# Kernel tuning notes

Measured on AMD Instinct MI355X. Metric: run time of the kernel, lower is better.

Reference implementation:

```python
import jax, jax.numpy as jnp
import numpy as np

N = 100000; E = 200000; H = 64; P2 = 250000; P3 = 500000; G = 2048; NC = 10
NF = 18; EF = 18; Y = 0.25; EPS_BN = 1e-5


def setup_inputs() -> dict:
    key = jax.random.key(0)
    ks = jax.random.split(key, 20)
    def rn(i, shape, s=0.05):
        return jax.random.normal(ks[i], shape, jnp.float32) * s
    inp = {}
    inp["x"] = jax.random.normal(ks[0], (N, NF), jnp.float32)
    inp["edge_attr"] = jax.random.normal(ks[1], (E, EF), jnp.float32)
    inp["paths2"] = jax.random.randint(ks[2], (P2, 2), 0, N, jnp.int32)
    inp["ei2"] = jax.random.randint(ks[3], (P2, 1), 0, E, jnp.int32)
    inp["paths3"] = jax.random.randint(ks[4], (P3, 3), 0, N, jnp.int32)
    inp["ei3"] = jax.random.randint(ks[5], (P3, 2), 0, E, jnp.int32)
    inp["batch"] = jnp.sort(jax.random.randint(ks[6], (N,), 0, G, jnp.int32))
    inp["w_feat"] = rn(7, (NF, H)); inp["b_feat"] = jnp.zeros((H,), jnp.float32)
    inp["w_bond"] = rn(8, (EF, H)); inp["b_bond"] = jnp.zeros((H,), jnp.float32)
    inp["w_ih"] = rn(9, (4 * H, 2 * H)); inp["w_hh"] = rn(10, (4 * H, H))
    inp["b_ih"] = jnp.zeros((4 * H,), jnp.float32); inp["b_hh"] = jnp.zeros((4 * H,), jnp.float32)
    inp["bn_g"] = jnp.ones((2, H), jnp.float32); inp["bn_b"] = jnp.zeros((2, H), jnp.float32)
    inp["mlp_w1"] = rn(11, (2, H, H)); inp["mlp_b1"] = jnp.zeros((2, H), jnp.float32)
    inp["bn1_g"] = jnp.ones((2, H), jnp.float32); inp["bn1_b"] = jnp.zeros((2, H), jnp.float32)
    inp["mlp_w2"] = rn(12, (2, H, H)); inp["mlp_b2"] = jnp.zeros((2, H), jnp.float32)
    inp["bn2_g"] = jnp.ones((2, H), jnp.float32); inp["bn2_b"] = jnp.zeros((2, H), jnp.float32)
    inp["w_att"] = rn(13, (H,)); inp["b_att"] = jnp.zeros((1,), jnp.float32)
    inp["w_l1"] = rn(14, (H, H)); inp["b_l1"] = jnp.zeros((H,), jnp.float32)
    inp["w_l2"] = rn(15, (H, NC)); inp["b_l2"] = jnp.zeros((NC,), jnp.float32)
    return inp


def _batch_norm(x, g, b):
    # training-mode BN: biased batch statistics, eps=1e-5 (torch BatchNorm1d)
    m = x.mean(axis=0)
    v = x.var(axis=0)
    return (x - m) * jax.lax.rsqrt(v + EPS_BN) * g + b


def _lstm_final(x_seq, w_ih, w_hh, b_ih, b_hh):
    # x_seq: [P, L, 2H]; torch LSTM gate order i,f,g,o; return final hidden [P, H]
    P = x_seq.shape[0]
    Hd = w_hh.shape[1]
    def step(carry, xt):
        h, c = carry
        gates = xt @ w_ih.T + b_ih + h @ w_hh.T + b_hh
        i, f, g, o = jnp.split(gates, 4, axis=-1)
        c = jax.nn.sigmoid(f) * c + jax.nn.sigmoid(i) * jnp.tanh(g)
        h = jax.nn.sigmoid(o) * jnp.tanh(c)
        return (h, c), None
    h0 = jnp.zeros((P, Hd), x_seq.dtype)
    (h, _), _ = jax.lax.scan(step, (h0, h0), jnp.swapaxes(x_seq, 0, 1))
    return h


def _conv(i, x_in, ea_enc, paths, ei, w_ih, w_hh, b_ih, b_hh, bn_g, bn_b,
          mlp_w1, mlp_b1, bn1_g, bn1_b, mlp_w2, mlp_b2, bn2_g, bn2_b):
    P = paths.shape[0]
    ea = ea_enc[ei]                                        # [P, L-1, H]
    ea = jnp.concatenate([jnp.zeros((P, 1, H), ea.dtype), ea], axis=1)  # [P, L, H]
    x_cat = jnp.concatenate([x_in[paths], ea], axis=-1)    # [P, L, 2H]
    h = _lstm_final(x_cat, w_ih, w_hh, b_ih, b_hh)         # [P, H]
    h = jax.ops.segment_sum(h, paths[:, -1], num_segments=N)  # scatter_add to nodes
    h = _batch_norm(h, bn_g[i], bn_b[i])                   # residuals=False
    h = jax.nn.relu(_batch_norm(h @ mlp_w1[i] + mlp_b1[i], bn1_g[i], bn1_b[i]))
    h = jax.nn.relu(_batch_norm(h @ mlp_w2[i] + mlp_b2[i], bn2_g[i], bn2_b[i]))
    return h


def _attention(query, keys, w_att, b_att):
    scores = []
    for k in keys:
        s = jnp.sum(query * k, axis=0)                     # [H], sum over nodes
        s = (s - s.min()) / (s.max() - s.min() + 1e-6)
        scores.append(s @ w_att + b_att[0])                # scalar
    w = jax.nn.softmax(jnp.stack(scores))                  # [K]
    rep = sum(k * w[j] for j, k in enumerate(keys))
    return rep + query


def _forward(x, edge_attr, w_feat, b_feat, w_bond, b_bond, w_ih, w_hh, b_ih, b_hh,
             bn_g, bn_b, mlp_w1, mlp_b1, bn1_g, bn1_b, mlp_w2, mlp_b2, bn2_g, bn2_b,
             w_att, b_att, w_l1, b_l1, w_l2, b_l2, paths2, ei2, paths3, ei3, batch):
    W0 = x @ w_feat + b_feat                               # [N, H]
    ea_enc = edge_attr @ w_bond + b_bond                   # [E, H]
    common = (w_ih, w_hh, b_ih, b_hh, bn_g, bn_b, mlp_w1, mlp_b1, bn1_g, bn1_b,
              mlp_w2, mlp_b2, bn2_g, bn2_b)
    W1 = _conv(0, W0, ea_enc, paths2, ei2, *common)
    Win = (1.0 - Y) * W0 - Y * W1
    W2 = _conv(1, Win, ea_enc, paths3, ei3, *common)
    out = _attention(W0, [W1, W2], w_att, b_att)           # [N, H]
    out = jax.ops.segment_sum(out, batch, num_segments=G)  # global_add_pool -> [G, H]
    out = jax.nn.relu(out @ w_l1 + b_l1)
    return out @ w_l2 + b_l2                               # [G, NC]


def reference(x, edge_attr, paths2, ei2, paths3, ei3, batch, w_feat, b_feat,
              w_bond, b_bond, w_ih, w_hh, b_ih, b_hh, bn_g, bn_b, mlp_w1, mlp_b1,
              bn1_g, bn1_b, mlp_w2, mlp_b2, bn2_g, bn2_b, w_att, b_att,
              w_l1, b_l1, w_l2, b_l2):
    return _forward(x, edge_attr, w_feat, b_feat, w_bond, b_bond, w_ih, w_hh, b_ih, b_hh,
                    bn_g, bn_b, mlp_w1, mlp_b1, bn1_g, bn1_b, mlp_w2, mlp_b2, bn2_g, bn2_b,
                    w_att, b_att, w_l1, b_l1, w_l2, b_l2, paths2, ei2, paths3, ei3, batch)
```

## Files before the change

### kernel.cpp

```cpp
#include <hip/hip_runtime.h>
#include <math.h>

#define NNODES 100000
#define NEDGES 200000
#define HD 64
#define NP2 250000
#define NP3 500000
#define NG 2048
#define NCLS 10
#define NFEAT 18
#define EFEAT 18

typedef short short8v __attribute__((ext_vector_type(8)));
typedef float f32x4 __attribute__((ext_vector_type(4)));

__device__ __forceinline__ unsigned short bf16r(float a) {
    unsigned u = __builtin_bit_cast(unsigned, a);
    return (unsigned short)((u + 0x7FFFu + ((u >> 16) & 1u)) >> 16);
}

#define LOG2E 1.4426950408889634f

__global__ void prep_all(const float* __restrict__ w_ih, const float* __restrict__ w_hh,
                         const float* __restrict__ b_ih, const float* __restrict__ b_hh,
                         unsigned short* __restrict__ Bp, float* __restrict__ bsum,
                         float* __restrict__ zsmall, float* __restrict__ pooled) {
    int b = blockIdx.x;
    int t = threadIdx.x;
    if (b < 192) {
        int gid = b * 256 + t;
        int kc = gid >> 13;
        int rem = gid & 8191;
        int nt = rem >> 9;
        int rem2 = rem & 511;
        int l = rem2 >> 3, j = rem2 & 7;
        int c = l & 15, q = l >> 4;
        int jh = nt >> 2, qg = nt & 3;
        int k = kc * 32 + q * 8 + j;
        int n = qg * 64 + 16 * jh + c;
        float f = (k < 128) ? w_ih[n * 128 + k] : w_hh[n * 64 + (k - 128)];
        float s = (qg == 2) ? 2.f * LOG2E : LOG2E;
        Bp[gid] = bf16r(f * s);
    } else if (b == 192) {
        float s = ((t >> 6) == 2) ? 2.f * LOG2E : LOG2E;
        bsum[t] = (b_ih[t] + b_hh[t]) * s;
        for (int i = t; i < 960; i += 256) zsmall[i] = 0.f;
    } else {
        pooled[(b - 193) * 256 + t] = 0.f;
    }
}

__global__ void encode_all(const float* __restrict__ X, const float* __restrict__ Wf,
                           const float* __restrict__ bf,
                           const float* __restrict__ Ea, const float* __restrict__ Wb,
                           const float* __restrict__ bb,
                           float* __restrict__ W0, unsigned short* __restrict__ W0b,
                           unsigned short* __restrict__ eab) {
    long gid = (long)blockIdx.x * 256 + threadIdx.x;
    if (gid >= (long)(NNODES + NEDGES) * 64) return;
    long r = gid >> 6;
    int col = (int)(gid & 63);
    if (r < NNODES) {
        float acc = bf[col];
        const float* xr = X + r * NFEAT;
        for (int k = 0; k < NFEAT; ++k) acc += xr[k] * Wf[k * 64 + col];
        W0[gid] = acc;
        W0b[gid] = bf16r(acc);
    } else {
        long r2 = r - NNODES;
        float acc = bb[col];
        const float* xr = Ea + r2 * EFEAT;
        for (int k = 0; k < EFEAT; ++k) acc += xr[k] * Wb[k * 64 + col];
        eab[r2 * 64 + col] = bf16r(acc);
    }
}

template <int L>
__global__ __launch_bounds__(256, 3)
void conv_mfma(const unsigned short* __restrict__ xb, const unsigned short* __restrict__ eab,
               const int* __restrict__ paths, const int* __restrict__ ei,
               const unsigned short* __restrict__ Bp, const float* __restrict__ bsum,
               float* __restrict__ hsum, int P) {
    __shared__ unsigned short Al[2][64 * 200];
    __shared__ int lastnode_s[64];

    const int t = threadIdx.x;
    const int w = t >> 6, lane = t & 63;
    const int c = lane & 15, q = lane >> 4;
    const int pl = t >> 2, gq = t & 3;
    const long pg = (long)blockIdx.x * 64 + pl;
    const int pc = (pg < P) ? (int)pg : P - 1;

    const short8v* __restrict__ Bv = (const short8v*)Bp;
    const int bbase = w * 256 + lane;

    float breg[4];
#pragma unroll
    for (int g2 = 0; g2 < 4; ++g2) breg[g2] = bsum[g2 * 64 + 16 * w + c];

    float creg[16];
#pragma unroll
    for (int i = 0; i < 16; ++i) creg[i] = 0.f;

    f32x4 acc[4][4];
    short8v bs0[4], bs1[4], bs2[4];
    uint4 nu0, nu1, ev0, ev1;

    {
        int node = paths[pc * L + 0];
        const uint4* s4 = (const uint4*)(xb + (size_t)node * HD);
        *(uint4*)&Al[0][pl * 200 + gq * 16] = s4[2 * gq];
        *(uint4*)&Al[0][pl * 200 + gq * 16 + 8] = s4[2 * gq + 1];
        if (gq == 0) lastnode_s[pl] = paths[pc * L + (L - 1)];
    }
    __syncthreads();

#define LOADB(BUF, KC)                                                         \
        { _Pragma("unroll")                                                    \
          for (int g2 = 0; g2 < 4; ++g2)                                       \
              BUF[g2] = Bv[(KC) * 1024 + g2 * 64 + bbase]; }

#define CHUNKS(BUF, KC)                                                        \
        { _Pragma("unroll")                                                    \
          for (int mt = 0; mt < 4; ++mt) {                                     \
              short8v af = *(const short8v*)&Ac[(mt * 16 + c) * 200 + (KC) * 32 + q * 8]; \
              _Pragma("unroll")                                                \
              for (int g2 = 0; g2 < 4; ++g2)                                   \
                  acc[mt][g2] = __builtin_amdgcn_mfma_f32_16x16x32_bf16(       \
                      af, BUF[g2], acc[mt][g2], 0, 0, 0);                      \
          } }

    int cur = 0;
    for (int step = 0; step < L; ++step) {
        const unsigned short* Ac = Al[cur];
        unsigned short* An = Al[cur ^ 1];

#pragma unroll
        for (int mt = 0; mt < 4; ++mt)
#pragma unroll
            for (int g2 = 0; g2 < 4; ++g2) {
                f32x4 v; v[0] = breg[g2]; v[1] = breg[g2]; v[2] = breg[g2]; v[3] = breg[g2];
                acc[mt][g2] = v;
            }

        if (step == 0) {
            LOADB(bs0, 0)
            LOADB(bs1, 1)
            {
                int node = paths[pc * L + 1];
                const uint4* s4 = (const uint4*)(xb + (size_t)node * HD);
                nu0 = s4[2 * gq]; nu1 = s4[2 * gq + 1];
                int e = ei[pc * (L - 1) + 0];
                const uint4* e4 = (const uint4*)(eab + (size_t)e * HD);
                ev0 = e4[2 * gq]; ev1 = e4[2 * gq + 1];
            }
            CHUNKS(bs0, 0)
            CHUNKS(bs1, 1)
        } else {
            LOADB(bs0, 0) LOADB(bs1, 1) LOADB(bs2, 2)
            CHUNKS(bs0, 0) LOADB(bs0, 3)
            CHUNKS(bs1, 1) LOADB(bs1, 4)
            CHUNKS(bs2, 2) LOADB(bs2, 5)
            if (step + 1 < L) {
                int node = paths[pc * L + step + 1];
                const uint4* s4 = (const uint4*)(xb + (size_t)node * HD);
                nu0 = s4[2 * gq]; nu1 = s4[2 * gq + 1];
                int e = ei[pc * (L - 1) + step];
                const uint4* e4 = (const uint4*)(eab + (size_t)e * HD);
                ev0 = e4[2 * gq]; ev1 = e4[2 * gq + 1];
            }
            CHUNKS(bs0, 3)
            CHUNKS(bs1, 4)
            CHUNKS(bs2, 5)
        }

#pragma unroll
        for (int mt = 0; mt < 4; ++mt) {
#pragma unroll
            for (int r = 0; r < 4; ++r) {
                float gi = acc[mt][0][r], gf = acc[mt][1][r];
                float gg = acc[mt][2][r], go = acc[mt][3][r];
                float ea = __builtin_amdgcn_exp2f(-gf);
                float eb = __builtin_amdgcn_exp2f(-gi);
                float ed = __builtin_amdgcn_exp2f(-gg);
                float eo = __builtin_amdgcn_exp2f(-go);
                float pa = 1.f + ea, pb = 1.f + eb, pd = 1.f + ed;
                float cn = (creg[mt * 4 + r] * pb * pd + (1.f - ed) * pa) *
                           __builtin_amdgcn_rcpf(pa * pb * pd);
                creg[mt * 4 + r] = cn;
                float et = __builtin_amdgcn_exp2f(-2.8853900817779268f * cn);
                float hn = (1.f - et) *
                           __builtin_amdgcn_rcpf((1.f + eo) * (1.f + et));
                if (step < L - 1) {
                    An[(mt * 16 + q * 4 + r) * 200 + 128 + 16 * w + c] = bf16r(hn);
                } else {
                    long pr = (long)blockIdx.x * 64 + mt * 16 + q * 4 + r;
                    if (pr < P) {
                        int node = lastnode_s[mt * 16 + q * 4 + r];
                        atomicAdd(hsum + (size_t)node * HD + 16 * w + c, hn);
                    }
                }
            }
        }

        if (step + 1 < L) {
            *(uint4*)&An[pl * 200 + gq * 16] = nu0;
            *(uint4*)&An[pl * 200 + gq * 16 + 8] = nu1;
            *(uint4*)&An[pl * 200 + 64 + gq * 16] = ev0;
            *(uint4*)&An[pl * 200 + 64 + gq * 16 + 8] = ev1;
            __syncthreads();
        }
        cur ^= 1;
    }
#undef LOADB
#undef CHUNKS
}

__global__ void col_stats(const float* __restrict__ X, int nrows, float* __restrict__ out) {
    int col = threadIdx.x & 63, rg = threadIdx.x >> 6;
    float s = 0.f, q = 0.f;
    long stride = (long)gridDim.x * 4;
    for (long r = (long)blockIdx.x * 4 + rg; r < nrows; r += stride) {
        float v = X[r * 64 + col];
        s += v;
        q += v * v;
    }
    __shared__ float red[2][256];
    red[0][threadIdx.x] = s;
    red[1][threadIdx.x] = q;
    __syncthreads();
    if (threadIdx.x < 64) {
        int c = threadIdx.x;
        float ss = red[0][c] + red[0][c + 64] + red[0][c + 128] + red[0][c + 192];
        float qq = red[1][c] + red[1][c + 64] + red[1][c + 128] + red[1][c + 192];
        atomicAdd(out + c, ss);
        atomicAdd(out + 64 + c, qq);
    }
}

__device__ __forceinline__ void bn_affine(const float* stats, const float* g,
                                          const float* b, int col, int nrows,
                                          float& a, float& c) {
    float inv = 1.0f / (float)nrows;
    float mean = stats[col] * inv;
    float var = stats[64 + col] * inv - mean * mean;
    a = g[col] * rsqrtf(var + 1e-5f);
    c = b[col] - mean * a;
}

template <bool INRELU, bool STATS>
__global__ __launch_bounds__(256)
void gemm64(const float* __restrict__ X, const float* __restrict__ stats_in,
            const float* __restrict__ bn_gm, const float* __restrict__ bn_bt,
            const float* __restrict__ W, const float* __restrict__ bias,
            float* __restrict__ Y, float* stats, int nrows) {
    __shared__ float Xs[64 * 64];
    __shared__ float red[2][256];
    const int t = threadIdx.x;
    const int col = t & 63, rg = t >> 6;
    const long r0 = (long)blockIdx.x * 64;

    float a = 1.f, c = 0.f;
    if (stats_in) bn_affine(stats_in, bn_gm, bn_bt, col, nrows, a, c);

    for (int i = 0; i < 16; ++i) {
        int rl = rg * 16 + i;
        long r = r0 + rl;
        float v = (r < nrows) ? X[r * 64 + col] : 0.f;
        v = v * a + c;
        if (INRELU) v = fmaxf(v, 0.f);
        Xs[rl * 64 + col] = v;
    }
    __syncthreads();

    float wreg[64];
#pragma unroll
    for (int k = 0; k < 64; ++k) wreg[k] = W[k * 64 + col];
    float bs = bias[col];
    float ssum = 0.f, ssq = 0.f;

    for (int i = 0; i < 16; ++i) {
        int rl = rg * 16 + i;
        long r = r0 + rl;
        const float4* xs4 = (const float4*)(Xs + rl * 64);
        float acc = bs;
#pragma unroll
        for (int k4 = 0; k4 < 16; ++k4) {
            float4 xv = xs4[k4];
            acc += xv.x * wreg[4 * k4] + xv.y * wreg[4 * k4 + 1] +
                   xv.z * wreg[4 * k4 + 2] + xv.w * wreg[4 * k4 + 3];
        }
        if (r < nrows) {
            Y[r * 64 + col] = acc;
            ssum += acc;
            ssq += acc * acc;
        }
    }
    if (STATS) {
        red[0][t] = ssum;
        red[1][t] = ssq;
        __syncthreads();
        if (t < 64) {
            float s = red[0][t] + red[0][t + 64] + red[0][t + 128] + red[0][t + 192];
            float qq = red[1][t] + red[1][t + 64] + red[1][t + 128] + red[1][t + 192];
            atomicAdd(stats + t, s);
            atomicAdd(stats + 64 + t, qq);
        }
    }
}

__global__ void bn_apply1(float* __restrict__ W1, const float* __restrict__ stats,
                          const float* __restrict__ g, const float* __restrict__ b,
                          const float* __restrict__ W0, unsigned short* __restrict__ Winb,
                          long n) {
    long gid = (long)blockIdx.x * 256 + threadIdx.x;
    if (gid >= n * 64) return;
    int col = (int)(gid & 63);
    float a, c;
    bn_affine(stats, g, b, col, (int)n, a, c);
    float v = fmaxf(W1[gid] * a + c, 0.f);
    W1[gid] = v;
    Winb[gid] = bf16r(0.75f * W0[gid] - 0.25f * v);
}

__global__ void bn_apply_att(float* __restrict__ W2, const float* __restrict__ stats,
                             const float* __restrict__ g, const float* __restrict__ b,
                             const float* __restrict__ W0, const float* __restrict__ W1,
                             float* __restrict__ atts, int n) {
    int col = threadIdx.x & 63, rg = threadIdx.x >> 6;
    float a, c;
    bn_affine(stats, g, b, col, n, a, c);
    float s1 = 0.f, s2 = 0.f;
    long stride = (long)gridDim.x * 4;
    for (long r = (long)blockIdx.x * 4 + rg; r < n; r += stride) {
        long gid = r * 64 + col;
        float v = fmaxf(W2[gid] * a + c, 0.f);
        W2[gid] = v;
        float q0 = W0[gid];
        s1 += q0 * W1[gid];
        s2 += q0 * v;
    }
    __shared__ float red[2][256];
    red[0][threadIdx.x] = s1;
    red[1][threadIdx.x] = s2;
    __syncthreads();
    if (threadIdx.x < 64) {
        int cc = threadIdx.x;
        float a1 = red[0][cc] + red[0][cc + 64] + red[0][cc + 128] + red[0][cc + 192];
        float a2 = red[1][cc] + red[1][cc + 64] + red[1][cc + 128] + red[1][cc + 192];
        atomicAdd(atts + cc, a1);
        atomicAdd(atts + 64 + cc, a2);
    }
}

#define PROWS 128
__global__ void pool_rep(const float* __restrict__ W0, const float* __restrict__ W1,
                         const float* __restrict__ W2, const float* __restrict__ atts,
                         const float* __restrict__ w_att, const float* __restrict__ b_att,
                         const int* __restrict__ batch, float* __restrict__ pooled, int n) {
    __shared__ float wsh[2];
    if (threadIdx.x < 64) {
        int h = threadIdx.x;
        float z[2];
        for (int k = 0; k < 2; ++k) {
            float s = atts[64 * k + h];
            float mn = s, mx = s;
            for (int off = 32; off > 0; off >>= 1) {
                mn = fminf(mn, __shfl_down(mn, off));
                mx = fmaxf(mx, __shfl_down(mx, off));
            }
            mn = __shfl(mn, 0);
            mx = __shfl(mx, 0);
            float sn = (s - mn) / (mx - mn + 1e-6f);
            float d = sn * w_att[h];
            for (int off = 32; off > 0; off >>= 1) d += __shfl_down(d, off);
            z[k] = __shfl(d, 0) + b_att[0];
        }
        if (h == 0) {
            float m = fmaxf(z[0], z[1]);
            float e0 = expf(z[0] - m), e1 = expf(z[1] - m);
            float inv = 1.0f / (e0 + e1);
            wsh[0] = e0 * inv;
            wsh[1] = e1 * inv;
        }
    }
    __syncthreads();
    int col = threadIdx.x & 63, rg = threadIdx.x >> 6;
    long r0 = (long)blockIdx.x * PROWS;
    float w1 = wsh[0], w2 = wsh[1];
    float acc = 0.f;
    int curg = -1;
    for (int i = rg; i < PROWS; i += 4) {
        long r = r0 + i;
        if (r >= n) break;
        int g = batch[r];
        long gid = r * 64 + col;
        float rep = W0[gid] + w1 * W1[gid] + w2 * W2[gid];
        if (g != curg) {
            if (curg >= 0) atomicAdd(pooled + (size_t)curg * 64 + col, acc);
            curg = g;
            acc = 0.f;
        }
        acc += rep;
    }
    if (curg >= 0) atomicAdd(pooled + (size_t)curg * 64 + col, acc);
}

__global__ __launch_bounds__(256)
void head_kernel(const float* __restrict__ pooled, const float* __restrict__ w_l1,
                 const float* __restrict__ b_l1, const float* __restrict__ w_l2,
                 const float* __restrict__ b_l2, float* __restrict__ out) {
    __shared__ float Xs[64 * 64];
    __shared__ float Ys[64 * 65];
    const int t = threadIdx.x;
    const int col = t & 63, rg = t >> 6;
    const int r0 = blockIdx.x * 64;

    for (int i = 0; i < 16; ++i) {
        int rl = rg * 16 + i;
        Xs[rl * 64 + col] = fmaxf(pooled[(size_t)(r0 + rl) * 64 + col], 0.f);
    }
    __syncthreads();

    float wreg[64];
#pragma unroll
    for (int k = 0; k < 64; ++k) wreg[k] = w_l1[k * 64 + col];
    float bs = b_l1[col];

    for (int i = 0; i < 16; ++i) {
        int rl = rg * 16 + i;
        const float4* xs4 = (const float4*)(Xs + rl * 64);
        float acc = bs;
#pragma unroll
        for (int k4 = 0; k4 < 16; ++k4) {
            float4 xv = xs4[k4];
            acc += xv.x * wreg[4 * k4] + xv.y * wreg[4 * k4 + 1] +
                   xv.z * wreg[4 * k4 + 2] + xv.w * wreg[4 * k4 + 3];
        }
        Ys[rl * 65 + col] = fmaxf(acc, 0.f);
    }
    __syncthreads();

    for (int idx = t; idx < 64 * NCLS; idx += 256) {
        int row = idx / NCLS, j = idx - row * NCLS;
        float acc = b_l2[j];
#pragma unroll
        for (int k = 0; k < 64; ++k) acc += Ys[row * 65 + k] * w_l2[k * NCLS + j];
        out[(size_t)(r0 + row) * NCLS + j] = acc;
    }
}

extern "C" void kernel_launch(void* const* d_in, const int* in_sizes, int n_in,
                              void* d_out, int out_size, void* d_ws, size_t ws_size,
                              hipStream_t stream) {
    const float* x         = (const float*)d_in[0];
    const float* edge_attr = (const float*)d_in[1];
    const int*   paths2    = (const int*)d_in[2];
    const int*   ei2       = (const int*)d_in[3];
    const int*   paths3    = (const int*)d_in[4];
    const int*   ei3       = (const int*)d_in[5];
    const int*   batch     = (const int*)d_in[6];
    const float* w_feat    = (const float*)d_in[7];
    const float* b_feat    = (const float*)d_in[8];
    const float* w_bond    = (const float*)d_in[9];
    const float* b_bond    = (const float*)d_in[10];
    const float* w_ih      = (const float*)d_in[11];
    const float* w_hh      = (const float*)d_in[12];
    const float* b_ih      = (const float*)d_in[13];
    const float* b_hh      = (const float*)d_in[14];
    const float* bn_g      = (const float*)d_in[15];
    const float* bn_b      = (const float*)d_in[16];
    const float* mlp_w1    = (const float*)d_in[17];
    const float* mlp_b1    = (const float*)d_in[18];
    const float* bn1_g     = (const float*)d_in[19];
    const float* bn1_b     = (const float*)d_in[20];
    const float* mlp_w2    = (const float*)d_in[21];
    const float* mlp_b2    = (const float*)d_in[22];
    const float* bn2_g     = (const float*)d_in[23];
    const float* bn2_b     = (const float*)d_in[24];
    const float* w_att     = (const float*)d_in[25];
    const float* b_att     = (const float*)d_in[26];
    const float* w_l1      = (const float*)d_in[27];
    const float* b_l1      = (const float*)d_in[28];
    const float* w_l2      = (const float*)d_in[29];
    const float* b_l2      = (const float*)d_in[30];

    const size_t N64 = (size_t)NNODES * 64;
    float* ws = (float*)d_ws;
    float* W0     = ws;
    float* W1     = W0 + N64;
    float* W2     = W1 + N64;
    float* Wtmp   = W2 + N64;
    float* hsum1  = Wtmp + N64;
    float* hsum2  = hsum1 + N64;
    unsigned short* W0b  = (unsigned short*)(hsum2 + N64);
    unsigned short* Winb = W0b + N64;
    unsigned short* eab  = Winb + N64;
    unsigned short* Bp   = eab + (size_t)NEDGES * 64;
    float* bsum   = (float*)(Bp + 6 * 16 * 64 * 8);
    float* st     = bsum + 256;
    float* atts   = st + 6 * 128;
    float* watt   = atts + 128;
    float* pooled = watt + 64;

    hipMemsetAsync(hsum1, 0, 2 * N64 * sizeof(float), stream);

    prep_all<<<193 + 512, 256, 0, stream>>>(w_ih, w_hh, b_ih, b_hh, Bp, bsum, st, pooled);
    encode_all<<<(int)(((size_t)(NNODES + NEDGES) * 64 + 255) / 256), 256, 0, stream>>>(
        x, w_feat, b_feat, edge_attr, w_bond, b_bond, W0, W0b, eab);

    conv_mfma<2><<<(NP2 + 63) / 64, 256, 0, stream>>>(W0b, eab, paths2, ei2, Bp, bsum, hsum1, NP2);

    col_stats<<<1024, 256, 0, stream>>>(hsum1, NNODES, st + 0);
    gemm64<false, true><<<(NNODES + 63) / 64, 256, 0, stream>>>(hsum1, st + 0, bn_g + 0, bn_b + 0, mlp_w1, mlp_b1, Wtmp, st + 128, NNODES);
    gemm64<true, true><<<(NNODES + 63) / 64, 256, 0, stream>>>(Wtmp, st + 128, bn1_g + 0, bn1_b + 0, mlp_w2, mlp_b2, W1, st + 256, NNODES);
    bn_apply1<<<(NNODES * 64 + 255) / 256, 256, 0, stream>>>(W1, st + 256, bn2_g + 0, bn2_b + 0, W0, Winb, NNODES);

    conv_mfma<3><<<(NP3 + 63) / 64, 256, 0, stream>>>(Winb, eab, paths3, ei3, Bp, bsum, hsum2, NP3);

    col_stats<<<1024, 256, 0, stream>>>(hsum2, NNODES, st + 384);
    gemm64<false, true><<<(NNODES + 63) / 64, 256, 0, stream>>>(hsum2, st + 384, bn_g + 64, bn_b + 64, mlp_w1 + 4096, mlp_b1 + 64, Wtmp, st + 512, NNODES);
    gemm64<true, true><<<(NNODES + 63) / 64, 256, 0, stream>>>(Wtmp, st + 512, bn1_g + 64, bn1_b + 64, mlp_w2 + 4096, mlp_b2 + 64, W2, st + 640, NNODES);
    bn_apply_att<<<1024, 256, 0, stream>>>(W2, st + 640, bn2_g + 64, bn2_b + 64, W0, W1, atts, NNODES);

    pool_rep<<<(NNODES + PROWS - 1) / PROWS, 256, 0, stream>>>(W0, W1, W2, atts, w_att, b_att, batch, pooled, NNODES);
    head_kernel<<<NG / 64, 256, 0, stream>>>(pooled, w_l1, b_l1, w_l2, b_l2, (float*)d_out);
}
```

Before: 718.0 us.

## Fuse post-conv BN/MLP/attention/pool/head chain into cooperative persistent kernels

Replaces the sequence of col_stats, two gemm64, bn_apply, attention, pooling and head launches after each conv with a single cooperative-launch kernel that uses grid.sync between phases. It also merges the hsum memset, weight prep and encoding into one launch. The aim is to remove many kernel launch gaps and tail effects. The cost is grid-wide barriers, a fixed 768-block grid that may underuse or over-subscribe the GPU, and register pressure from holding 64 weights per thread.

```diff
diff --git a/kernel.cpp b/kernel.cpp
--- a/kernel.cpp
+++ b/kernel.cpp
@@ -1,5 +1,8 @@
 #include <hip/hip_runtime.h>
+#include <hip/hip_cooperative_groups.h>
 #include <math.h>
+
+namespace cg = cooperative_groups;
 
 #define NNODES 100000
 #define NEDGES 200000
@@ -10,6 +13,7 @@
 #define NCLS 10
 #define NFEAT 18
 #define EFEAT 18
+#define GRID_MID 768
 
 typedef short short8v __attribute__((ext_vector_type(8)));
 typedef float f32x4 __attribute__((ext_vector_type(4)));
@@ -21,14 +25,41 @@
 
 #define LOG2E 1.4426950408889634f
 
-__global__ void prep_all(const float* __restrict__ w_ih, const float* __restrict__ w_hh,
-                         const float* __restrict__ b_ih, const float* __restrict__ b_hh,
-                         unsigned short* __restrict__ Bp, float* __restrict__ bsum,
-                         float* __restrict__ zsmall, float* __restrict__ pooled) {
+#define NB_ENC (((NNODES + NEDGES) * 64 + 255) / 256)
+
+__global__ void prep_encode(const float* __restrict__ X, const float* __restrict__ Wf,
+                            const float* __restrict__ bf,
+                            const float* __restrict__ Ea, const float* __restrict__ Wb,
+                            const float* __restrict__ bb,
+                            float* __restrict__ W0, unsigned short* __restrict__ W0b,
+                            unsigned short* __restrict__ eab,
+                            const float* __restrict__ w_ih, const float* __restrict__ w_hh,
+                            const float* __restrict__ b_ih, const float* __restrict__ b_hh,
+                            unsigned short* __restrict__ Bp, float* __restrict__ bsum,
+                            float* __restrict__ zsmall, float* __restrict__ hzero,
+                            float* __restrict__ pooled) {
     int b = blockIdx.x;
     int t = threadIdx.x;
-    if (b < 192) {
-        int gid = b * 256 + t;
+    if (b < NB_ENC) {
+        long gid = (long)b * 256 + t;
+        if (gid >= (long)(NNODES + NEDGES) * 64) return;
+        long r = gid >> 6;
+        int col = (int)(gid & 63);
+        if (r < NNODES) {
+            float acc = bf[col];
+            const float* xr = X + r * NFEAT;
+            for (int k = 0; k < NFEAT; ++k) acc += xr[k] * Wf[k * 64 + col];
+            W0[gid] = acc;
+            W0b[gid] = bf16r(acc);
+        } else {
+            long r2 = r - NNODES;
+            float acc = bb[col];
+            const float* xr = Ea + r2 * EFEAT;
+            for (int k = 0; k < EFEAT; ++k) acc += xr[k] * Wb[k * 64 + col];
+            eab[r2 * 64 + col] = bf16r(acc);
+        }
+    } else if (b < NB_ENC + 192) {
+        int gid = (b - NB_ENC) * 256 + t;
         int kc = gid >> 13;
         int rem = gid & 8191;
         int nt = rem >> 9;
@@ -41,37 +72,18 @@
         float f = (k < 128) ? w_ih[n * 128 + k] : w_hh[n * 64 + (k - 128)];
         float s = (qg == 2) ? 2.f * LOG2E : LOG2E;
         Bp[gid] = bf16r(f * s);
-    } else if (b == 192) {
+    } else if (b == NB_ENC + 192) {
         float s = ((t >> 6) == 2) ? 2.f * LOG2E : LOG2E;
         bsum[t] = (b_ih[t] + b_hh[t]) * s;
         for (int i = t; i < 960; i += 256) zsmall[i] = 0.f;
+    } else if (b < NB_ENC + 193 + 3200) {
+        long base = ((long)(b - NB_ENC - 193) * 256 + t) * 16;
+        f32x4 z = {0.f, 0.f, 0.f, 0.f};
+        f32x4* p = (f32x4*)(hzero + base);
+        long lim = 2L * NNODES * 64;
+        if (base + 16 <= lim) { p[0] = z; p[1] = z; p[2] = z; p[3] = z; }
     } else {
-        pooled[(b - 193) * 256 + t] = 0.f;
-    }
-}
-
-__global__ void encode_all(const float* __restrict__ X, const float* __restrict__ Wf,
-                           const float* __restrict__ bf,
-                           const float* __restrict__ Ea, const float* __restrict__ Wb,
-                           const float* __restrict__ bb,
-                           float* __restrict__ W0, unsigned short* __restrict__ W0b,
-                           unsigned short* __restrict__ eab) {
-    long gid = (long)blockIdx.x * 256 + threadIdx.x;
-    if (gid >= (long)(NNODES + NEDGES) * 64) return;
-    long r = gid >> 6;
-    int col = (int)(gid & 63);
-    if (r < NNODES) {
-        float acc = bf[col];
-        const float* xr = X + r * NFEAT;
-        for (int k = 0; k < NFEAT; ++k) acc += xr[k] * Wf[k * 64 + col];
-        W0[gid] = acc;
-        W0b[gid] = bf16r(acc);
-    } else {
-        long r2 = r - NNODES;
-        float acc = bb[col];
-        const float* xr = Ea + r2 * EFEAT;
-        for (int k = 0; k < EFEAT; ++k) acc += xr[k] * Wb[k * 64 + col];
-        eab[r2 * 64 + col] = bf16r(acc);
+        pooled[(b - NB_ENC - 193 - 3200) * 256 + t] = 0.f;
     }
 }
 
@@ -192,7 +204,7 @@
                 float hn = (1.f - et) *
                            __builtin_amdgcn_rcpf((1.f + eo) * (1.f + et));
                 if (step < L - 1) {
-                    An[(mt * 16 + q * 4 + r) * 200 + 128 + 16 * w + c] = bf16r(hn);
+                    Al[cur ^ 1][(mt * 16 + q * 4 + r) * 200 + 128 + 16 * w + c] = bf16r(hn);
                 } else {
                     long pr = (long)blockIdx.x * 64 + mt * 16 + q * 4 + r;
                     if (pr < P) {
@@ -214,6 +226,245 @@
     }
 #undef LOADB
 #undef CHUNKS
+}
+
+__device__ __forceinline__ void bn_affine(const float* stats, const float* g,
+                                          const float* b, int col, int nrows,
+                                          float& a, float& c) {
+    float inv = 1.0f / (float)nrows;
+    float mean = stats[col] * inv;
+    float var = stats[64 + col] * inv - mean * mean;
+    a = g[col] * rsqrtf(var + 1e-5f);
+    c = b[col] - mean * a;
+}
+
+template <bool INRELU>
+__device__ __forceinline__ void gemm_phase(
+    const float* __restrict__ X, const float* __restrict__ stats_in,
+    const float* __restrict__ bn_gm, const float* __restrict__ bn_bt,
+    const float* __restrict__ W, const float* __restrict__ bias,
+    float* __restrict__ Y, float* __restrict__ stats,
+    float* Xs, float* red0, float* red1, int t, int col, int rg) {
+    float a, c;
+    bn_affine(stats_in, bn_gm, bn_bt, col, NNODES, a, c);
+    float wreg[64];
+#pragma unroll
+    for (int k = 0; k < 64; ++k) wreg[k] = W[k * 64 + col];
+    float bs = bias[col];
+    float ssum = 0.f, ssq = 0.f;
+    const int NT = (NNODES + 63) / 64;
+    for (int tile = blockIdx.x; tile < NT; tile += gridDim.x) {
+        long r0 = (long)tile * 64;
+        for (int i = 0; i < 16; ++i) {
+            int rl = rg * 16 + i;
+            long r = r0 + rl;
+            float v = (r < NNODES) ? X[r * 64 + col] : 0.f;
+            v = v * a + c;
+            if (INRELU) v = fmaxf(v, 0.f);
+            Xs[rl * 64 + col] = v;
+        }
+        __syncthreads();
+        for (int i = 0; i < 16; ++i) {
+            int rl = rg * 16 + i;
+            long r = r0 + rl;
+            const float4* xs4 = (const float4*)(Xs + rl * 64);
+            float acc = bs;
+#pragma unroll
+            for (int k4 = 0; k4 < 16; ++k4) {
+                float4 xv = xs4[k4];
+                acc += xv.x * wreg[4 * k4] + xv.y * wreg[4 * k4 + 1] +
+                       xv.z * wreg[4 * k4 + 2] + xv.w * wreg[4 * k4 + 3];
+            }
+            if (r < NNODES) {
+                Y[r * 64 + col] = acc;
+                ssum += acc;
+                ssq += acc * acc;
+            }
+        }
+        __syncthreads();
+    }
+    red0[t] = ssum;
+    red1[t] = ssq;
+    __syncthreads();
+    if (t < 64) {
+        float s = red0[t] + red0[t + 64] + red0[t + 128] + red0[t + 192];
+        float qq = red1[t] + red1[t + 64] + red1[t + 128] + red1[t + 192];
+        atomicAdd(stats + t, s);
+        atomicAdd(stats + 64 + t, qq);
+    }
+}
+
+template <int MODE>
+__global__ __launch_bounds__(256, 4)
+void midchain(const float* __restrict__ hsum,
+              const float* __restrict__ bng, const float* __restrict__ bnb,
+              const float* __restrict__ w1m, const float* __restrict__ b1m,
+              const float* __restrict__ bn1g, const float* __restrict__ bn1b,
+              const float* __restrict__ w2m, const float* __restrict__ b2m,
+              const float* __restrict__ bn2g, const float* __restrict__ bn2b,
+              float* __restrict__ Wtmp, float* __restrict__ Wout,
+              float* __restrict__ st,
+              const float* __restrict__ W0, const float* __restrict__ W1,
+              unsigned short* __restrict__ Winb,
+              float* __restrict__ atts,
+              const float* __restrict__ w_att, const float* __restrict__ b_att,
+              const int* __restrict__ batch, float* __restrict__ pooled,
+              const float* __restrict__ w_l1, const float* __restrict__ b_l1,
+              const float* __restrict__ w_l2, const float* __restrict__ b_l2,
+              float* __restrict__ out) {
+    cg::grid_group grid = cg::this_grid();
+    __shared__ float smem[64 * 64 + 64 * 65];
+    __shared__ float wsh[2];
+    float* Xs = smem;
+    float* red0 = smem + 4096;
+    float* red1 = smem + 4096 + 256;
+
+    const int t = threadIdx.x;
+    const int col = t & 63, rg = t >> 6;
+
+    {
+        float s = 0.f, q = 0.f;
+        long stride = (long)gridDim.x * 4;
+        for (long r = (long)blockIdx.x * 4 + rg; r < NNODES; r += stride) {
+            float v = hsum[r * 64 + col];
+            s += v;
+            q += v * v;
+        }
+        red0[t] = s;
+        red1[t] = q;
+        __syncthreads();
+        if (t < 64) {
+            float ss = red0[t] + red0[t + 64] + red0[t + 128] + red0[t + 192];
+            float qq = red1[t] + red1[t + 64] + red1[t + 128] + red1[t + 192];
+            atomicAdd(st + t, ss);
+            atomicAdd(st + 64 + t, qq);
+        }
+    }
+    grid.sync();
+
+    gemm_phase<false>(hsum, st, bng, bnb, w1m, b1m, Wtmp, st + 128, Xs, red0, red1, t, col, rg);
+    grid.sync();
+
+    gemm_phase<true>(Wtmp, st + 128, bn1g, bn1b, w2m, b2m, Wout, st + 256, Xs, red0, red1, t, col, rg);
+    grid.sync();
+
+    if (MODE == 0) {
+        float a, c;
+        bn_affine(st + 256, bn2g, bn2b, col, NNODES, a, c);
+        long stride = (long)gridDim.x * 256;
+        for (long gid = (long)blockIdx.x * 256 + t; gid < (long)NNODES * 64; gid += stride) {
+            float v = fmaxf(Wout[gid] * a + c, 0.f);
+            Wout[gid] = v;
+            Winb[gid] = bf16r(0.75f * W0[gid] - 0.25f * v);
+        }
+    } else {
+        float a, c;
+        bn_affine(st + 256, bn2g, bn2b, col, NNODES, a, c);
+        float s1 = 0.f, s2 = 0.f;
+        long stride = (long)gridDim.x * 4;
+        for (long r = (long)blockIdx.x * 4 + rg; r < NNODES; r += stride) {
+            long gid = r * 64 + col;
+            float v = fmaxf(Wout[gid] * a + c, 0.f);
+            Wout[gid] = v;
+            float q0 = W0[gid];
+            s1 += q0 * W1[gid];
+            s2 += q0 * v;
+        }
+        red0[t] = s1;
+        red1[t] = s2;
+        __syncthreads();
+        if (t < 64) {
+            float a1 = red0[t] + red0[t + 64] + red0[t + 128] + red0[t + 192];
+            float a2 = red1[t] + red1[t + 64] + red1[t + 128] + red1[t + 192];
+            atomicAdd(atts + t, a1);
+            atomicAdd(atts + 64 + t, a2);
+        }
+        grid.sync();
+
+        if (t < 64) {
+            int h = t;
+            float z[2];
+            for (int k = 0; k < 2; ++k) {
+                float s = atts[64 * k + h];
+                float mn = s, mx = s;
+                for (int off = 32; off > 0; off >>= 1) {
+                    mn = fminf(mn, __shfl_down(mn, off));
+                    mx = fmaxf(mx, __shfl_down(mx, off));
+                }
+                mn = __shfl(mn, 0);
+                mx = __shfl(mx, 0);
+                float sn = (s - mn) / (mx - mn + 1e-6f);
+                float d = sn * w_att[h];
+                for (int off = 32; off > 0; off >>= 1) d += __shfl_down(d, off);
+                z[k] = __shfl(d, 0) + b_att[0];
+            }
+            if (h == 0) {
+                float m = fmaxf(z[0], z[1]);
+                float e0 = expf(z[0] - m), e1 = expf(z[1] - m);
+                float inv = 1.0f / (e0 + e1);
+                wsh[0] = e0 * inv;
+                wsh[1] = e1 * inv;
+            }
+        }
+        __syncthreads();
+        float w1a = wsh[0], w2a = wsh[1];
+        const int NPT = (NNODES + 127) / 128;
+        for (int tile = blockIdx.x; tile < NPT; tile += gridDim.x) {
+            long r0p = (long)tile * 128;
+            float acc = 0.f;
+            int curg = -1;
+            for (int i = rg; i < 128; i += 4) {
+                long r = r0p + i;
+                if (r >= NNODES) break;
+                int g = batch[r];
+                long gid = r * 64 + col;
+                float rep = W0[gid] + w1a * W1[gid] + w2a * Wout[gid];
+                if (g != curg) {
+                    if (curg >= 0) atomicAdd(pooled + (size_t)curg * 64 + col, acc);
+                    curg = g;
+                    acc = 0.f;
+                }
+                acc += rep;
+            }
+            if (curg >= 0) atomicAdd(pooled + (size_t)curg * 64 + col, acc);
+        }
+        grid.sync();
+
+        float* Ys = smem + 4096;
+        float wreg[64];
+#pragma unroll
+        for (int k = 0; k < 64; ++k) wreg[k] = w_l1[k * 64 + col];
+        float bs = b_l1[col];
+        for (int tile = blockIdx.x; tile < NG / 64; tile += gridDim.x) {
+            int r0h = tile * 64;
+            for (int i = 0; i < 16; ++i) {
+                int rl = rg * 16 + i;
+                Xs[rl * 64 + col] = fmaxf(pooled[(size_t)(r0h + rl) * 64 + col], 0.f);
+            }
+            __syncthreads();
+            for (int i = 0; i < 16; ++i) {
+                int rl = rg * 16 + i;
+                const float4* xs4 = (const float4*)(Xs + rl * 64);
+                float acc = bs;
+#pragma unroll
+                for (int k4 = 0; k4 < 16; ++k4) {
+                    float4 xv = xs4[k4];
+                    acc += xv.x * wreg[4 * k4] + xv.y * wreg[4 * k4 + 1] +
+                           xv.z * wreg[4 * k4 + 2] + xv.w * wreg[4 * k4 + 3];
+                }
+                Ys[rl * 65 + col] = fmaxf(acc, 0.f);
+            }
+            __syncthreads();
+            for (int idx = t; idx < 64 * NCLS; idx += 256) {
+                int row = idx / NCLS, j = idx - row * NCLS;
+                float acc = b_l2[j];
+#pragma unroll
+                for (int k = 0; k < 64; ++k) acc += Ys[row * 65 + k] * w_l2[k * NCLS + j];
+                out[(size_t)(r0h + row) * NCLS + j] = acc;
+            }
+            __syncthreads();
+        }
+    }
 }
 
 __global__ void col_stats(const float* __restrict__ X, int nrows, float* __restrict__ out) {
@@ -236,16 +487,6 @@
         atomicAdd(out + c, ss);
         atomicAdd(out + 64 + c, qq);
     }
-}
-
-__device__ __forceinline__ void bn_affine(const float* stats, const float* g,
-                                          const float* b, int col, int nrows,
-                                          float& a, float& c) {
-    float inv = 1.0f / (float)nrows;
-    float mean = stats[col] * inv;
-    float var = stats[64 + col] * inv - mean * mean;
-    a = g[col] * rsqrtf(var + 1e-5f);
-    c = b[col] - mean * a;
 }
 
 template <bool INRELU, bool STATS>
@@ -502,27 +743,81 @@
     float* atts   = st + 6 * 128;
     float* watt   = atts + 128;
     float* pooled = watt + 64;
-
-    hipMemsetAsync(hsum1, 0, 2 * N64 * sizeof(float), stream);
-
-    prep_all<<<193 + 512, 256, 0, stream>>>(w_ih, w_hh, b_ih, b_hh, Bp, bsum, st, pooled);
-    encode_all<<<(int)(((size_t)(NNODES + NEDGES) * 64 + 255) / 256), 256, 0, stream>>>(
-        x, w_feat, b_feat, edge_attr, w_bond, b_bond, W0, W0b, eab);
+    float* outp   = (float*)d_out;
+
+    prep_encode<<<NB_ENC + 193 + 3200 + 512, 256, 0, stream>>>(
+        x, w_feat, b_feat, edge_attr, w_bond, b_bond, W0, W0b, eab,
+        w_ih, w_hh, b_ih, b_hh, Bp, bsum, st, hsum1, pooled);
 
     conv_mfma<2><<<(NP2 + 63) / 64, 256, 0, stream>>>(W0b, eab, paths2, ei2, Bp, bsum, hsum1, NP2);
 
-    col_stats<<<1024, 256, 0, stream>>>(hsum1, NNODES, st + 0);
-    gemm64<false, true><<<(NNODES + 63) / 64, 256, 0, stream>>>(hsum1, st + 0, bn_g + 0, bn_b + 0, mlp_w1, mlp_b1, Wtmp, st + 128, NNODES);
-    gemm64<true, true><<<(NNODES + 63) / 64, 256, 0, stream>>>(Wtmp, st + 128, bn1_g + 0, bn1_b + 0, mlp_w2, mlp_b2, W1, st + 256, NNODES);
-    bn_apply1<<<(NNODES * 64 + 255) / 256, 256, 0, stream>>>(W1, st + 256, bn2_g + 0, bn2_b + 0, W0, Winb, NNODES);
+    {
+        const float* a_hsum = hsum1;
+        const float* a_bng = bn_g;         const float* a_bnb = bn_b;
+        const float* a_w1m = mlp_w1;       const float* a_b1m = mlp_b1;
+        const float* a_bn1g = bn1_g;       const float* a_bn1b = bn1_b;
+        const float* a_w2m = mlp_w2;       const float* a_b2m = mlp_b2;
+        const float* a_bn2g = bn2_g;       const float* a_bn2b = bn2_b;
+        float* a_Wtmp = Wtmp;              float* a_Wout = W1;
+        float* a_st = st;
+        const float* a_W0 = W0;            const float* a_W1 = nullptr;
+        unsigned short* a_Winb = Winb;
+        float* a_atts = atts;
+        const float* a_watt = w_att;       const float* a_batt = b_att;
+        const int* a_batch = batch;        float* a_pooled = pooled;
+        const float* a_wl1 = w_l1;         const float* a_bl1 = b_l1;
+        const float* a_wl2 = w_l2;         const float* a_bl2 = b_l2;
+        float* a_out = outp;
+        void* args[] = {&a_hsum, &a_bng, &a_bnb, &a_w1m, &a_b1m, &a_bn1g, &a_bn1b,
+                        &a_w2m, &a_b2m, &a_bn2g, &a_bn2b, &a_Wtmp, &a_Wout, &a_st,
+                        &a_W0, &a_W1, &a_Winb, &a_atts, &a_watt, &a_batt,
+                        &a_batch, &a_pooled, &a_wl1, &a_bl1, &a_wl2, &a_bl2, &a_out};
+        auto kfn = midchain<0>;
+        hipError_t ce = hipLaunchCooperativeKernel((const void*)kfn, dim3(GRID_MID),
+                                                   dim3(256), args, 0, stream);
+        if (ce != hipSuccess) {
+            (void)hipGetLastError();
+            col_stats<<<1024, 256, 0, stream>>>(hsum1, NNODES, st + 0);
+            gemm64<false, true><<<(NNODES + 63) / 64, 256, 0, stream>>>(hsum1, st + 0, bn_g, bn_b, mlp_w1, mlp_b1, Wtmp, st + 128, NNODES);
+            gemm64<true, true><<<(NNODES + 63) / 64, 256, 0, stream>>>(Wtmp, st + 128, bn1_g, bn1_b, mlp_w2, mlp_b2, W1, st + 256, NNODES);
+            bn_apply1<<<(int)((N64 + 255) / 256), 256, 0, stream>>>(W1, st + 256, bn2_g, bn2_b, W0, Winb, NNODES);
+        }
+    }
 
     conv_mfma<3><<<(NP3 + 63) / 64, 256, 0, stream>>>(Winb, eab, paths3, ei3, Bp, bsum, hsum2, NP3);
 
-    col_stats<<<1024, 256, 0, stream>>>(hsum2, NNODES, st + 384);
-    gemm64<false, true><<<(NNODES + 63) / 64, 256, 0, stream>>>(hsum2, st + 384, bn_g + 64, bn_b + 64, mlp_w1 + 4096, mlp_b1 + 64, Wtmp, st + 512, NNODES);
-    gemm64<true, true><<<(NNODES + 63) / 64, 256, 0, stream>>>(Wtmp, st + 512, bn1_g + 64, bn1_b + 64, mlp_w2 + 4096, mlp_b2 + 64, W2, st + 640, NNODES);
-    bn_apply_att<<<1024, 256, 0, stream>>>(W2, st + 640, bn2_g + 64, bn2_b + 64, W0, W1, atts, NNODES);
-
-    pool_rep<<<(NNODES + PROWS - 1) / PROWS, 256, 0, stream>>>(W0, W1, W2, atts, w_att, b_att, batch, pooled, NNODES);
-    head_kernel<<<NG / 64, 256, 0, stream>>>(pooled, w_l1, b_l1, w_l2, b_l2, (float*)d_out);
-}
+    {
+        const float* a_hsum = hsum2;
+        const float* a_bng = bn_g + 64;    const float* a_bnb = bn_b + 64;
+        const float* a_w1m = mlp_w1 + 4096; const float* a_b1m = mlp_b1 + 64;
+        const float* a_bn1g = bn1_g + 64;  const float* a_bn1b = bn1_b + 64;
+        const float* a_w2m = mlp_w2 + 4096; const float* a_b2m = mlp_b2 + 64;
+        const float* a_bn2g = bn2_g + 64;  const float* a_bn2b = bn2_b + 64;
+        float* a_Wtmp = Wtmp;              float* a_Wout = W2;
+        float* a_st = st + 384;
+        const float* a_W0 = W0;            const float* a_W1 = W1;
+        unsigned short* a_Winb = Winb;
+        float* a_atts = atts;
+        const float* a_watt = w_att;       const float* a_batt = b_att;
+        const int* a_batch = batch;        float* a_pooled = pooled;
+        const float* a_wl1 = w_l1;         const float* a_bl1 = b_l1;
+        const float* a_wl2 = w_l2;         const float* a_bl2 = b_l2;
+        float* a_out = outp;
+        void* args[] = {&a_hsum, &a_bng, &a_bnb, &a_w1m, &a_b1m, &a_bn1g, &a_bn1b,
+                        &a_w2m, &a_b2m, &a_bn2g, &a_bn2b, &a_Wtmp, &a_Wout, &a_st,
+                        &a_W0, &a_W1, &a_Winb, &a_atts, &a_watt, &a_batt,
+                        &a_batch, &a_pooled, &a_wl1, &a_bl1, &a_wl2, &a_bl2, &a_out};
+        auto kfn = midchain<1>;
+        hipError_t ce = hipLaunchCooperativeKernel((const void*)kfn, dim3(GRID_MID),
+                                                   dim3(256), args, 0, stream);
+        if (ce != hipSuccess) {
+            (void)hipGetLastError();
+            col_stats<<<1024, 256, 0, stream>>>(hsum2, NNODES, st + 384);
+            gemm64<false, true><<<(NNODES + 63) / 64, 256, 0, stream>>>(hsum2, st + 384, bn_g + 64, bn_b + 64, mlp_w1 + 4096, mlp_b1 + 64, Wtmp, st + 512, NNODES);
+            gemm64<true, true><<<(NNODES + 63) / 64, 256, 0, stream>>>(Wtmp, st + 512, bn1_g + 64, bn1_b + 64, mlp_w2 + 4096, mlp_b2 + 64, W2, st + 640, NNODES);
+            bn_apply_att<<<1024, 256, 0, stream>>>(W2, st + 640, bn2_g + 64, bn2_b + 64, W0, W1, atts, NNODES);
+            pool_rep<<<(NNODES + PROWS - 1) / PROWS, 256, 0, stream>>>(W0, W1, W2, atts, w_att, b_att, batch, pooled, NNODES);
+            head_kernel<<<NG / 64, 256, 0, stream>>>(pooled, w_l1, b_l1, w_l2, b_l2, outp);
+        }
+    }
+}
```

Measured after the change: 1.259 ms. 1.75x slower.
